# Kernel tuning notes

Measured on AMD Instinct MI355X. Metric: run time of the kernel, lower is better.

The kernel has to match this reference:

```python
import jax, jax.numpy as jnp
import numpy as np

RPN_BATCHSIZE = 256
RPN_FG_FRACTION = 0.5
STRIDE = 16
NEG_OVERLAP = 0.3
POS_OVERLAP = 0.7
ALLOWED_BORDER = 0.0


def _base_anchors(base_size=16, ratios=(0.5, 1.0, 2.0), scales=(8, 16, 32)):
    cx = cy = (base_size - 1) / 2.0
    size = float(base_size * base_size)
    out = []
    for r in ratios:
        ws = round(np.sqrt(size / r))
        hs = round(ws * r)
        for s in scales:
            W, H = ws * s, hs * s
            out.append([cx - (W - 1) / 2.0, cy - (H - 1) / 2.0,
                        cx + (W - 1) / 2.0, cy + (H - 1) / 2.0])
    return jnp.asarray(np.array(out, dtype=np.float32))


def _all_anchors(rr, cc, stride):
    # keras_rcnn.backend.shift((rr, cc), stride) -> (rr*cc*9, 4)
    base = _base_anchors()
    sx = jnp.arange(rr, dtype=jnp.float32) * stride
    sy = jnp.arange(cc, dtype=jnp.float32) * stride
    SX, SY = jnp.meshgrid(sx, sy)  # 'xy' indexing as in keras-rcnn
    shifts = jnp.stack([SX.ravel(), SY.ravel(), SX.ravel(), SY.ravel()], axis=1)
    return (shifts[:, None, :] + base[None, :, :]).reshape(-1, 4)


def _overlap(a, b):
    # pairwise IoU with the +1 pixel convention; a: (N,4), b: (G,4) -> (N,G)
    area_a = (a[:, 2] - a[:, 0] + 1.0) * (a[:, 3] - a[:, 1] + 1.0)
    area_b = (b[:, 2] - b[:, 0] + 1.0) * (b[:, 3] - b[:, 1] + 1.0)
    iw = jnp.maximum(jnp.minimum(a[:, None, 2], b[None, :, 2]) - jnp.maximum(a[:, None, 0], b[None, :, 0]) + 1.0, 0.0)
    ih = jnp.maximum(jnp.minimum(a[:, None, 3], b[None, :, 3]) - jnp.maximum(a[:, None, 1], b[None, :, 1]) + 1.0, 0.0)
    inter = iw * ih
    return inter / (area_a[:, None] + area_b[None, :] - inter)


def _bbox_transform(ex, gt):
    # keras_rcnn.backend.bbox_transform: (dx, dy, dw, dh) with +1 convention
    ew = ex[:, 2] - ex[:, 0] + 1.0
    eh = ex[:, 3] - ex[:, 1] + 1.0
    ecx = ex[:, 0] + 0.5 * ew
    ecy = ex[:, 1] + 0.5 * eh
    gw = gt[:, 2] - gt[:, 0] + 1.0
    gh = gt[:, 3] - gt[:, 1] + 1.0
    gcx = gt[:, 0] + 0.5 * gw
    gcy = gt[:, 1] + 0.5 * gh
    return jnp.stack([(gcx - ecx) / ew, (gcy - ecy) / eh,
                      jnp.log(gw / ew), jnp.log(gh / eh)], axis=1)


def _subsample(labels, value, max_keep, key):
    # randomly demote labels==value to -1 (don't care) so at most max_keep remain;
    # jit-friendly equivalent of shuffle + scatter in the original.
    mask = labels == value
    r = jnp.where(mask, jax.random.uniform(key, labels.shape), -1.0)
    rank = jnp.argsort(jnp.argsort(-r))  # rank 0 = highest random score
    keep = jnp.minimum(jnp.sum(mask), max_keep)
    return jnp.where(mask & (rank >= keep), -1.0, labels)


def _anchor_target(scores, gt_boxes, metadata):
    meta = metadata[0]          # (height, width, scale)
    gt = gt_boxes[0]            # (G, 4)
    rr, cc = scores.shape[1], scores.shape[2]
    anchors = _all_anchors(rr, cc, STRIDE)  # (N, 4)
    inside = ((anchors[:, 0] >= -ALLOWED_BORDER) & (anchors[:, 1] >= -ALLOWED_BORDER)
              & (anchors[:, 2] < ALLOWED_BORDER + meta[1])
              & (anchors[:, 3] < ALLOWED_BORDER + meta[0]))
    overlaps = _overlap(anchors, gt)                     # (N, G)
    overlaps = jnp.where(inside[:, None], overlaps, -1.0)
    argmax_inds = jnp.argmax(overlaps, axis=1)           # best gt per anchor
    max_ov = jnp.take_along_axis(overlaps, argmax_inds[:, None], axis=1)[:, 0]
    gt_argmax = jnp.argmax(overlaps, axis=0)             # best anchor per gt
    labels = jnp.full((anchors.shape[0],), -1.0, dtype=jnp.float32)
    # clobber_positives=False: negatives first
    labels = jnp.where(inside & (max_ov < NEG_OVERLAP), 0.0, labels)
    # unique + scatter_add in the original just sets these entries to 1
    labels = labels.at[gt_argmax].set(1.0)
    labels = jnp.where(max_ov >= POS_OVERLAP, 1.0, labels)
    # balance: at most 128 positives, then fill to 256 with negatives
    k1, k2 = jax.random.split(jax.random.key(42))
    labels = _subsample(labels, 1.0, int(RPN_FG_FRACTION * RPN_BATCHSIZE), k1)
    n_pos = jnp.sum(labels == 1.0)
    labels = _subsample(labels, 0.0, RPN_BATCHSIZE - n_pos, k2)
    targets = _bbox_transform(anchors, gt[argmax_inds])
    targets = jnp.where(inside[:, None], targets, 0.0)   # unmap with fill=0
    return labels[None, :], targets[None, :, :]


def setup_inputs() -> dict:
    key = jax.random.key(0)
    k1, k2, k3 = jax.random.split(key, 3)
    scores = jax.random.normal(k1, (1, 128, 128, 18), dtype=jnp.float32)
    # valid GT boxes inside a 2048x2048 image: x1<x2, y1<y2
    xy = jax.random.uniform(k2, (1, 128, 2), minval=0.0, maxval=1800.0)
    wh = jax.random.uniform(k3, (1, 128, 2), minval=16.0, maxval=240.0)
    gt_boxes = jnp.concatenate([xy, xy + wh], axis=-1)
    metadata = jnp.ones((1, 3), dtype=jnp.float32) * jnp.array([2048.0, 2048.0, 1.0], dtype=jnp.float32)
    return {"scores": scores, "gt_boxes": gt_boxes, "metadata": metadata}


def reference(scores, gt_boxes, metadata):
    return _anchor_target(scores, gt_boxes, metadata)
```

## Files before the change

### kernel.cpp

```cpp
#include <hip/hip_runtime.h>
#include <stdint.h>

#define N_ANCH 147456
#define NGT 128

#define W_CNTS   0
#define W_SEL    1152
#define W_GMAX2  1160
#define W_LCNT   3208
#define W_LIST   4360
#define MAXSURV  2048

__constant__ float c_base[9][4] = {
  {-84.f,-40.f,99.f,55.f},
  {-176.f,-88.f,191.f,103.f},
  {-360.f,-184.f,375.f,199.f},
  {-56.f,-56.f,71.f,71.f},
  {-120.f,-120.f,135.f,135.f},
  {-248.f,-248.f,263.f,263.f},
  {-36.f,-80.f,51.f,95.f},
  {-80.f,-168.f,95.f,183.f},
  {-168.f,-344.f,183.f,359.f},
};
__constant__ float c_areaA[9] = {
  17664.f, 70656.f, 282624.f,
  16384.f, 65536.f, 262144.f,
  15488.f, 61952.f, 247808.f,
};

__host__ __device__ inline uint32_t rotl32(uint32_t v, int d){ return (v<<d)|(v>>(32-d)); }

__host__ __device__ inline void tf2x32(uint32_t k0, uint32_t k1, uint32_t x0, uint32_t x1,
                                       uint32_t* o0, uint32_t* o1){
  uint32_t ks0=k0, ks1=k1, ks2=k0^k1^0x1BD11BDAu;
  x0 += ks0; x1 += ks1;
  #define TFR(r) { x0 += x1; x1 = rotl32(x1,(r)); x1 ^= x0; }
  TFR(13) TFR(15) TFR(26) TFR(6)   x0+=ks1; x1+=ks2+1u;
  TFR(17) TFR(29) TFR(16) TFR(24)  x0+=ks2; x1+=ks0+2u;
  TFR(13) TFR(15) TFR(26) TFR(6)   x0+=ks0; x1+=ks1+3u;
  TFR(17) TFR(29) TFR(16) TFR(24)  x0+=ks1; x1+=ks2+4u;
  TFR(13) TFR(15) TFR(26) TFR(6)   x0+=ks2; x1+=ks0+5u;
  #undef TFR
  *o0=x0; *o1=x1;
}

__device__ inline uint32_t rand_m23(uint32_t k0, uint32_t k1, uint32_t j){
  uint32_t a, b;
  tf2x32(k0, k1, 0u, j, &a, &b);
  return (a ^ b) >> 9;
}

__global__ __launch_bounds__(256) void kA(const float* __restrict__ gt,
                                          const float* __restrict__ meta,
                                          signed char* __restrict__ lab,
                                          uint32_t* __restrict__ keys,
                                          uint32_t* __restrict__ ctl,
                                          float* __restrict__ out,
                                          uint32_t pk0,uint32_t pk1,
                                          uint32_t nk0,uint32_t nk1){
  int bid = blockIdx.x;
  float W = meta[1], H = meta[0];
  if (bid < 576){
    __shared__ float4 sg[NGT];
    __shared__ float  sB[NGT];
    __shared__ uint32_t slist[NGT];
    __shared__ unsigned long long sball[2];
    __shared__ uint32_t cpk;
    if (threadIdx.x == 0) cpk = 0u;
    for (int t = threadIdx.x; t < NGT; t += 256){
      float4 G = reinterpret_cast<const float4*>(gt)[t];
      sg[t] = G;
      sB[t] = __fmul_rn(G.z - G.x + 1.0f, G.w - G.y + 1.0f);
    }
    int i0 = bid*256, k0 = i0/9, k1 = (i0+255)/9;
    int y0 = k0 >> 7, y1 = k1 >> 7;
    int x0 = (y0==y1) ? (k0 & 127) : 0, x1 = (y0==y1) ? (k1 & 127) : 127;
    float Rxlo = 16.f*x0 - 361.f, Rxhi = 16.f*x1 + 376.f;
    float Rylo = 16.f*y0 - 345.f, Ryhi = 16.f*y1 + 360.f;
    __syncthreads();
    if (threadIdx.x < NGT){
      float4 G = sg[threadIdx.x];
      bool rel = (G.x <= Rxhi) && (G.z >= Rxlo) && (G.y <= Ryhi) && (G.w >= Rylo);
      unsigned long long b = __ballot(rel);
      if ((threadIdx.x & 63) == 0) sball[threadIdx.x >> 6] = b;
    }
    __syncthreads();
    unsigned long long b0 = sball[0], b1 = sball[1];
    if (threadIdx.x < NGT){
      float4 G = sg[threadIdx.x];
      bool rel = (G.x <= Rxhi) && (G.z >= Rxlo) && (G.y <= Ryhi) && (G.w >= Rylo);
      if (rel){
        int lane = threadIdx.x & 63;
        unsigned long long my = (threadIdx.x < 64) ? b0 : b1;
        uint32_t pos = (uint32_t)__popcll(my & ((1ull << lane) - 1ull));
        if (threadIdx.x >= 64) pos += (uint32_t)__popcll(b0);
        slist[pos] = (uint32_t)threadIdx.x;
      }
    }
    __syncthreads();
    int nl = (int)(__popcll(b0) + __popcll(b1));
    int fs;
    {
      unsigned long long n0 = ~b0;
      if (n0) fs = __ffsll((long long)n0) - 1;
      else { unsigned long long n1 = ~b1; fs = n1 ? 64 + __ffsll((long long)n1) - 1 : 128; }
    }
    int i = bid*256 + threadIdx.x;
    int k = i / 9; int t9 = i - k*9;
    float sx = 16.0f * (float)(k & 127);
    float sy = 16.0f * (float)(k >> 7);
    float ax1 = c_base[t9][0] + sx, ay1 = c_base[t9][1] + sy;
    float ax2 = c_base[t9][2] + sx, ay2 = c_base[t9][3] + sy;
    float areaA = c_areaA[t9];
    bool inside = (ax1 >= 0.0f) && (ay1 >= 0.0f) && (ax2 < W) && (ay2 < H);
    float best = -1.0f; int arg = 0;
    if (inside){
      best = -2.0f;
      for (int li = 0; li < nl; ++li){
        int g = (int)slist[li];
        float4 G = sg[g];
        float iw = fminf(ax2,G.z) - fmaxf(ax1,G.x) + 1.0f;
        float ih = fminf(ay2,G.w) - fmaxf(ay1,G.y) + 1.0f;
        float ov = 0.0f;
        if (iw > 0.0f && ih > 0.0f){
          float inter = __fmul_rn(iw, ih);
          ov = inter / ((areaA + sB[g]) - inter);
        }
        if (ov > best){ best = ov; arg = g; }
      }
      if (best < 0.0f){ best = 0.0f; arg = fs; }
      else if (best == 0.0f){ arg = (arg < fs) ? arg : fs; }
    }
    signed char L = -1;
    if (best >= 0.7f) L = 1;
    else if (inside && best < 0.3f) L = 0;
    lab[i] = L;
    if (L == 1) keys[i] = rand_m23(pk0,pk1,(uint32_t)i);
    else if (L == 0) keys[i] = rand_m23(nk0,nk1,(uint32_t)i);
    unsigned long long q1 = __ballot(L == 1);
    unsigned long long q0 = __ballot(L == 0);
    if ((threadIdx.x & 63) == 0){
      uint32_t add = ((uint32_t)__popcll(q1) << 16) | (uint32_t)__popcll(q0);
      if (add) atomicAdd(&cpk, add);
    }
    float4 t4 = make_float4(0.f, 0.f, 0.f, 0.f);
    if (inside){
      float4 G = sg[arg];
      float ew = ax2-ax1+1.0f, eh = ay2-ay1+1.0f;
      float ecx = ax1 + 0.5f*ew, ecy = ay1 + 0.5f*eh;
      float gw = G.z-G.x+1.0f, gh = G.w-G.y+1.0f;
      float gcx = G.x + 0.5f*gw, gcy = G.y + 0.5f*gh;
      t4.x = (gcx-ecx)/ew; t4.y = (gcy-ecy)/eh;
      t4.z = logf(gw/ew);  t4.w = logf(gh/eh);
    }
    *reinterpret_cast<float4*>(out + N_ANCH + 4*(size_t)i) = t4;
    __syncthreads();
    if (threadIdx.x == 0){
      uint32_t v = cpk;
      ctl[W_CNTS + 2*bid]     = v >> 16;
      ctl[W_CNTS + 2*bid + 1] = v & 0xFFFFu;
    }
  } else {
    int b2 = bid - 576;
    int g = b2 >> 3, slice = b2 & 7;
    float bx1=gt[4*g], by1=gt[4*g+1], bx2=gt[4*g+2], by2=gt[4*g+3];
    float areaB = __fmul_rn(bx2-bx1+1.0f, by2-by1+1.0f);
    int pxl = max(0,   (int)ceilf ((bx1 - 377.0f) * 0.0625f));
    int pxh = min(127, (int)floorf((bx2 + 362.0f) * 0.0625f));
    int pyl = max(0,   (int)ceilf ((by1 - 361.0f) * 0.0625f));
    int pyh = min(127, (int)floorf((by2 + 346.0f) * 0.0625f));
    uint32_t Wp = (uint32_t)(pxh - pxl + 1);
    int tot = (int)Wp * (pyh - pyl + 1);
    uint32_t mdiv = (4194304u + Wp - 1u) / Wp;
    float a0[9],a1[9],a2[9],a3[9];
    #pragma unroll
    for (int t=0;t<9;++t){ a0[t]=c_base[t][0]; a1[t]=c_base[t][1];
                           a2[t]=c_base[t][2]; a3[t]=c_base[t][3]; }
    float best = -2.0f; int bi = 0;
    for (int pos = slice*256 + threadIdx.x; pos < tot; pos += 2048){
      uint32_t dq = (uint32_t)(((unsigned long long)(uint32_t)pos * mdiv) >> 22);
      int py = pyl + (int)dq;
      int px = pxl + (int)((uint32_t)pos - dq * Wp);
      int k = (py << 7) + px;
      float sx = 16.0f * (float)px;
      float sy = 16.0f * (float)py;
      #pragma unroll
      for (int t = 0; t < 9; ++t){
        float ax1=a0[t]+sx, ay1=a1[t]+sy, ax2=a2[t]+sx, ay2=a3[t]+sy;
        bool inside = (ax1 >= 0.0f) && (ay1 >= 0.0f) && (ax2 < W) && (ay2 < H);
        float iw = fminf(ax2,bx2) - fmaxf(ax1,bx1) + 1.0f;
        float ih = fminf(ay2,by2) - fmaxf(ay1,by1) + 1.0f;
        float ov = inside ? 0.0f : -1.0f;
        if (inside && iw > 0.0f && ih > 0.0f){
          float inter = __fmul_rn(iw, ih);
          ov = inter / ((c_areaA[t] + areaB) - inter);
        }
        if (ov > best){ best = ov; bi = k*9 + t; }
      }
    }
    unsigned long long p = 0ull;
    if (best >= 0.0f)
      p = ((unsigned long long)__float_as_uint(best) << 32) | (uint32_t)(~(uint32_t)bi);
    __shared__ unsigned long long sred[256];
    sred[threadIdx.x] = p;
    __syncthreads();
    for (int s = 128; s > 0; s >>= 1){
      if ((int)threadIdx.x < s){
        unsigned long long q = sred[threadIdx.x + s];
        if (q > sred[threadIdx.x]) sred[threadIdx.x] = q;
      }
      __syncthreads();
    }
    if (threadIdx.x == 0)
      reinterpret_cast<unsigned long long*>(ctl + W_GMAX2)[b2] = sred[0];
  }
}

__global__ __launch_bounds__(256) void kC(const signed char* __restrict__ lab,
                                          const uint32_t* __restrict__ keys,
                                          float* __restrict__ out,
                                          uint32_t* __restrict__ ctl,
                                          uint32_t pk0, uint32_t pk1){
  int tid = threadIdx.x, bid = blockIdx.x;
  __shared__ uint32_t widx[NGT], wkey[NGT], wflag[256];
  __shared__ int sdP, sdN;
  __shared__ unsigned long long red[256];
  __shared__ uint32_t sel[6];
  __shared__ uint32_t lcnt[2];
  wflag[tid] = 0xFFFFFFFFu;
  if (tid == 0){ sdP = 0; sdN = 0; lcnt[0] = 0u; lcnt[1] = 0u; }
  if (tid < NGT){
    const unsigned long long* g2 =
      reinterpret_cast<const unsigned long long*>(ctl + W_GMAX2);
    unsigned long long best = 0ull;
    #pragma unroll
    for (int s = 0; s < 8; ++s){
      unsigned long long q = g2[tid*8 + s];
      if (q > best) best = q;
    }
    uint32_t idx = best ? ~(uint32_t)best : 0xFFFFFFFFu;
    widx[tid] = idx;
    wkey[tid] = (idx != 0xFFFFFFFFu) ? rand_m23(pk0, pk1, idx) : 0u;
  }
  unsigned long long acc = 0ull;
  for (int b = tid; b < 576; b += 256)
    acc += ((unsigned long long)ctl[W_CNTS + 2*b] << 32) | ctl[W_CNTS + 2*b + 1];
  red[tid] = acc;
  __syncthreads();
  for (int s = 128; s > 0; s >>= 1){
    if (tid < s) red[tid] += red[tid + s];
    __syncthreads();
  }
  if (tid < NGT && widx[tid] != 0xFFFFFFFFu){
    uint32_t idx = widx[tid];
    if ((idx >> 8) == (uint32_t)bid) wflag[idx & 255u] = wkey[tid];
    bool resp = true;
    for (int g = 0; g < tid; ++g) if (widx[g] == idx){ resp = false; break; }
    if (resp){
      int oldL = lab[idx];
      if (oldL != 1){ atomicAdd(&sdP, 1); if (oldL == 0) atomicAdd(&sdN, 1); }
    }
  }
  __syncthreads();
  if (tid == 0){
    uint32_t cntP = (uint32_t)(red[0] >> 32) + (uint32_t)sdP;
    uint32_t cntN = (uint32_t)red[0] - (uint32_t)sdN;
    uint32_t keepP = cntP < 128u ? cntP : 128u;
    uint32_t keepN = cntN < (256u - keepP) ? cntN : (256u - keepP);
    uint32_t cnts[2] = {cntP, cntN}, keeps[2] = {keepP, keepN};
    for (int c = 0; c < 2; ++c){
      uint32_t cnt = cnts[c], keep = keeps[c];
      uint32_t all = (keep >= cnt) ? 1u : 0u, Tf = 0u;
      if (!all){
        unsigned long long slack = 2ull * keep;
        if (slack < cnt)
          Tf = (uint32_t)((((unsigned long long)(cnt - slack)) << 23) / cnt);
      }
      sel[c*3+0] = Tf; sel[c*3+1] = keep; sel[c*3+2] = all;
    }
    if (bid == 0){
      for (int c = 0; c < 2; ++c){
        ctl[W_SEL + c*4 + 0] = sel[c*3+0];
        ctl[W_SEL + c*4 + 1] = sel[c*3+1];
        ctl[W_SEL + c*4 + 2] = sel[c*3+2];
      }
    }
  }
  __syncthreads();
  int i = bid*256 + tid;
  int L = lab[i];
  uint32_t wf = wflag[tid];
  uint32_t m = 0u;
  if (wf != 0xFFFFFFFFu){ L = 1; m = wf; }
  else if (L >= 0) m = keys[i];
  if (L < 0){
    out[i] = -1.0f;
  } else {
    int ch = (L == 1) ? 0 : 1;
    if (sel[ch*3+2]){
      out[i] = (float)L;
    } else if (m < sel[ch*3+0]){
      out[i] = -1.0f;
    } else {
      uint32_t pos = atomicAdd(&lcnt[ch], 1u);
      reinterpret_cast<unsigned long long*>(ctl + W_LIST)
        [(ch*576 + bid)*256 + pos] =
        ((unsigned long long)(m ^ 0x7FFFFFu) << 32) | (uint32_t)i;
    }
  }
  __syncthreads();
  if (tid < 2) ctl[W_LCNT + tid*576 + bid] = lcnt[tid];
}

__global__ __launch_bounds__(1024) void kD(float* __restrict__ out,
                                           uint32_t* __restrict__ ctl){
  int tid = threadIdx.x;
  __shared__ unsigned long long skey[MAXSURV];
  __shared__ uint32_t scan[1024];
  for (int c = 0; c < 2; ++c){
    uint32_t keep    = ctl[W_SEL + c*4 + 1];
    uint32_t keepAll = ctl[W_SEL + c*4 + 2];
    if (!keepAll){
      uint32_t cnum = (tid < 576) ? ctl[W_LCNT + c*576 + tid] : 0u;
      scan[tid] = cnum;
      __syncthreads();
      for (int off = 1; off < 1024; off <<= 1){
        uint32_t v = (tid >= off) ? scan[tid - off] : 0u;
        __syncthreads();
        scan[tid] += v;
        __syncthreads();
      }
      int n = (int)scan[1023]; if (n > MAXSURV) n = MAXSURV;
      if (cnum){
        uint32_t base = scan[tid] - cnum;
        const unsigned long long* list =
          reinterpret_cast<const unsigned long long*>(ctl + W_LIST)
          + (size_t)(c*576 + tid)*256;
        for (uint32_t j = 0; j < cnum; ++j){
          uint32_t p = base + j;
          if (p < (uint32_t)MAXSURV) skey[p] = list[j];
        }
      }
      __syncthreads();
      float kv = (c == 0) ? 1.0f : 0.0f;
      for (int p = tid; p < n; p += 1024){
        unsigned long long mine = skey[p];
        uint32_t r = 0;
        for (int j = 0; j < n; ++j) r += (skey[j] < mine) ? 1u : 0u;
        uint32_t idx = (uint32_t)(mine & 0xFFFFFFFFull);
        out[idx] = (r < keep) ? kv : -1.0f;
      }
    }
    __syncthreads();
  }
}

extern "C" void kernel_launch(void* const* d_in, const int* in_sizes, int n_in,
                              void* d_out, int out_size, void* d_ws, size_t ws_size,
                              hipStream_t stream) {
  const float* gt   = (const float*)d_in[1];
  const float* meta = (const float*)d_in[2];
  float* out = (float*)d_out;
  signed char* lab = (signed char*)d_ws;
  uint32_t* keys = (uint32_t*)((char*)d_ws + N_ANCH);
  uint32_t* ctl  = keys + N_ANCH;

  uint32_t a0,a1,b0,b1;
  tf2x32(0u, 42u, 0u, 0u, &a0, &a1);
  tf2x32(0u, 42u, 0u, 1u, &b0, &b1);

  kA<<<1600, 256, 0, stream>>>(gt, meta, lab, keys, ctl, out, a0, a1, b0, b1);
  kC<<<576, 256, 0, stream>>>(lab, keys, out, ctl, a0, a1);
  kD<<<1, 1024, 0, stream>>>(out, ctl);
}
```

Before: 47.72 us.

## Build per-wave GT relevance lists and halve GT-max slices per box

Result: faster. 45.33 us (-5.0%).

```diff
diff --git a/kernel.cpp b/kernel.cpp
--- a/kernel.cpp
+++ b/kernel.cpp
@@ -63,8 +63,7 @@
   if (bid < 576){
     __shared__ float4 sg[NGT];
     __shared__ float  sB[NGT];
-    __shared__ uint32_t slist[NGT];
-    __shared__ unsigned long long sball[2];
+    __shared__ uint32_t slist[4][NGT];
     __shared__ uint32_t cpk;
     if (threadIdx.x == 0) cpk = 0u;
     for (int t = threadIdx.x; t < NGT; t += 256){
@@ -72,39 +71,30 @@
       sg[t] = G;
       sB[t] = __fmul_rn(G.z - G.x + 1.0f, G.w - G.y + 1.0f);
     }
-    int i0 = bid*256, k0 = i0/9, k1 = (i0+255)/9;
-    int y0 = k0 >> 7, y1 = k1 >> 7;
-    int x0 = (y0==y1) ? (k0 & 127) : 0, x1 = (y0==y1) ? (k1 & 127) : 127;
+    __syncthreads();
+    int wv = threadIdx.x >> 6, lane = threadIdx.x & 63;
+    int i0w = bid*256 + wv*64;
+    int k0w = i0w/9, k1w = (i0w+63)/9;
+    int y0 = k0w >> 7, y1 = k1w >> 7;
+    int x0 = (y0==y1) ? (k0w & 127) : 0, x1 = (y0==y1) ? (k1w & 127) : 127;
     float Rxlo = 16.f*x0 - 361.f, Rxhi = 16.f*x1 + 376.f;
     float Rylo = 16.f*y0 - 345.f, Ryhi = 16.f*y1 + 360.f;
-    __syncthreads();
-    if (threadIdx.x < NGT){
-      float4 G = sg[threadIdx.x];
-      bool rel = (G.x <= Rxhi) && (G.z >= Rxlo) && (G.y <= Ryhi) && (G.w >= Rylo);
-      unsigned long long b = __ballot(rel);
-      if ((threadIdx.x & 63) == 0) sball[threadIdx.x >> 6] = b;
-    }
-    __syncthreads();
-    unsigned long long b0 = sball[0], b1 = sball[1];
-    if (threadIdx.x < NGT){
-      float4 G = sg[threadIdx.x];
-      bool rel = (G.x <= Rxhi) && (G.z >= Rxlo) && (G.y <= Ryhi) && (G.w >= Rylo);
-      if (rel){
-        int lane = threadIdx.x & 63;
-        unsigned long long my = (threadIdx.x < 64) ? b0 : b1;
-        uint32_t pos = (uint32_t)__popcll(my & ((1ull << lane) - 1ull));
-        if (threadIdx.x >= 64) pos += (uint32_t)__popcll(b0);
-        slist[pos] = (uint32_t)threadIdx.x;
-      }
-    }
-    __syncthreads();
-    int nl = (int)(__popcll(b0) + __popcll(b1));
+    float4 Ga = sg[lane], Gb = sg[lane+64];
+    bool r0 = (Ga.x <= Rxhi) && (Ga.z >= Rxlo) && (Ga.y <= Ryhi) && (Ga.w >= Rylo);
+    bool r1 = (Gb.x <= Rxhi) && (Gb.z >= Rxlo) && (Gb.y <= Ryhi) && (Gb.w >= Rylo);
+    unsigned long long m0 = __ballot(r0), m1 = __ballot(r1);
+    unsigned long long lt = (1ull << lane) - 1ull;
+    uint32_t c0n = (uint32_t)__popcll(m0);
+    if (r0) slist[wv][(uint32_t)__popcll(m0 & lt)] = (uint32_t)lane;
+    if (r1) slist[wv][c0n + (uint32_t)__popcll(m1 & lt)] = (uint32_t)(64 + lane);
+    int nl = (int)(c0n + (uint32_t)__popcll(m1));
     int fs;
     {
-      unsigned long long n0 = ~b0;
+      unsigned long long n0 = ~m0;
       if (n0) fs = __ffsll((long long)n0) - 1;
-      else { unsigned long long n1 = ~b1; fs = n1 ? 64 + __ffsll((long long)n1) - 1 : 128; }
-    }
+      else { unsigned long long n1 = ~m1; fs = n1 ? 64 + __ffsll((long long)n1) - 1 : 128; }
+    }
+    __syncthreads();
     int i = bid*256 + threadIdx.x;
     int k = i / 9; int t9 = i - k*9;
     float sx = 16.0f * (float)(k & 127);
@@ -117,7 +107,7 @@
     if (inside){
       best = -2.0f;
       for (int li = 0; li < nl; ++li){
-        int g = (int)slist[li];
+        int g = (int)slist[wv][li];
         float4 G = sg[g];
         float iw = fminf(ax2,G.z) - fmaxf(ax1,G.x) + 1.0f;
         float ih = fminf(ay2,G.w) - fmaxf(ay1,G.y) + 1.0f;
@@ -139,7 +129,7 @@
     else if (L == 0) keys[i] = rand_m23(nk0,nk1,(uint32_t)i);
     unsigned long long q1 = __ballot(L == 1);
     unsigned long long q0 = __ballot(L == 0);
-    if ((threadIdx.x & 63) == 0){
+    if (lane == 0){
       uint32_t add = ((uint32_t)__popcll(q1) << 16) | (uint32_t)__popcll(q0);
       if (add) atomicAdd(&cpk, add);
     }
@@ -162,7 +152,7 @@
     }
   } else {
     int b2 = bid - 576;
-    int g = b2 >> 3, slice = b2 & 7;
+    int g = b2 >> 2, slice = b2 & 3;
     float bx1=gt[4*g], by1=gt[4*g+1], bx2=gt[4*g+2], by2=gt[4*g+3];
     float areaB = __fmul_rn(bx2-bx1+1.0f, by2-by1+1.0f);
     int pxl = max(0,   (int)ceilf ((bx1 - 377.0f) * 0.0625f));
@@ -177,7 +167,7 @@
     for (int t=0;t<9;++t){ a0[t]=c_base[t][0]; a1[t]=c_base[t][1];
                            a2[t]=c_base[t][2]; a3[t]=c_base[t][3]; }
     float best = -2.0f; int bi = 0;
-    for (int pos = slice*256 + threadIdx.x; pos < tot; pos += 2048){
+    for (int pos = slice*256 + threadIdx.x; pos < tot; pos += 1024){
       uint32_t dq = (uint32_t)(((unsigned long long)(uint32_t)pos * mdiv) >> 22);
       int py = pyl + (int)dq;
       int px = pxl + (int)((uint32_t)pos - dq * Wp);
@@ -234,8 +224,8 @@
       reinterpret_cast<const unsigned long long*>(ctl + W_GMAX2);
     unsigned long long best = 0ull;
     #pragma unroll
-    for (int s = 0; s < 8; ++s){
-      unsigned long long q = g2[tid*8 + s];
+    for (int s = 0; s < 4; ++s){
+      unsigned long long q = g2[tid*4 + s];
       if (q > best) best = q;
     }
     uint32_t idx = best ? ~(uint32_t)best : 0xFFFFFFFFu;
@@ -369,7 +359,7 @@
   tf2x32(0u, 42u, 0u, 0u, &a0, &a1);
   tf2x32(0u, 42u, 0u, 1u, &b0, &b1);
 
-  kA<<<1600, 256, 0, stream>>>(gt, meta, lab, keys, ctl, out, a0, a1, b0, b1);
+  kA<<<1088, 256, 0, stream>>>(gt, meta, lab, keys, ctl, out, a0, a1, b0, b1);
   kC<<<576, 256, 0, stream>>>(lab, keys, out, ctl, a0, a1);
   kD<<<1, 1024, 0, stream>>>(out, ctl);
 }
```
